# Kernel optimization log

Measured on AMD Instinct MI355X. Metric: run time of the kernel, lower is better.

The kernel has to match this reference:

```python
import jax, jax.numpy as jnp
import numpy as np

B, N, C, H = 2, 384, 256, 4
D = C // H


def setup_inputs() -> dict:
    key = jax.random.key(0)
    k1, k2 = jax.random.split(key)
    x = jax.random.normal(k1, (B, N, C), dtype=jnp.float32)
    # nn.Linear(dim, 8*dim, bias=False) weight, scaled like default torch init magnitude
    W = jax.random.normal(k2, (8 * C, C), dtype=jnp.float32) / np.float32(np.sqrt(C))
    return {"x": x, "W": W}


def reference(x, W):
    Bx, Nx, Cx = x.shape
    Hh = H
    Dd = Cx // Hh
    scale = Dd ** -0.5
    # w(x): [B,N,8C] -> [B,N,8,H,D] -> [8,B,H,N,D]
    w = (x @ W.T).reshape(Bx, Nx, 8, Hh, Dd).transpose(2, 0, 3, 1, 4)
    a, b, c = w[0], w[1], w[2]          # w[3..5] (d,e,f) are unused in the torch forward
    v1, v2 = w[6], w[7]
    # pairwise logits, each [B,H,N,N]
    eAB = jnp.exp(jnp.einsum('bhid,bhjd->bhij', a, b) * scale)  # indexed [i,j]
    eCD = jnp.exp(jnp.einsum('bhid,bhjd->bhij', b, c) * scale)  # indexed [i,k]
    eEF = jnp.exp(jnp.einsum('bhid,bhjd->bhij', c, a) * scale)  # indexed [j,k]
    # exact factorization of exp(AB[ij]+CD[ik]+EF[jk]):
    # num[i,d] = sum_j eAB[ij] v1[jd] * (sum_k eCD[ik] eEF[jk] v2[kd])
    T = eEF[..., None] * v2[:, :, None, :, :]                   # [B,H,j,k,D]
    R = jnp.einsum('bhik,bhjkd->bhijd', eCD, T)                 # [B,H,i,j,D]
    num = jnp.einsum('bhij,bhjd,bhijd->bhid', eAB, v1, R)       # [B,H,N,D]
    den = jnp.sum(eAB * jnp.einsum('bhik,bhjk->bhij', eCD, eEF), axis=-1)  # [B,H,N]
    out = num / den[..., None]
    # [B,H,N,D] -> [B,N,H,D] -> [B,N,C]
    return out.transpose(0, 2, 1, 3).reshape(Bx, Nx, Cx)
```

## Files before the change

kernel.cpp:

```cpp
#include <hip/hip_runtime.h>
#include <math.h>

#define B_  2
#define N_  384
#define C_  256
#define H_  4
#define D_  64
#define NBH (B_*H_)
#define TSZ (NBH*N_*D_)
#define ESZ (NBH*N_*N_)
#define SCALE 0.125f

typedef _Float16 f16;
typedef f16  f16x8 __attribute__((ext_vector_type(8)));
typedef f16  f16x4 __attribute__((ext_vector_type(4)));
typedef float f32x4 __attribute__((ext_vector_type(4)));

__global__ __launch_bounds__(256) void proj_kernel(const float* __restrict__ x,
                                                   const float* __restrict__ W,
                                                   float* __restrict__ proj) {
    __shared__ float Xs[32][68];
    __shared__ float Ws[32][68];
    const int tid = threadIdx.x;
    const int tx = tid & 15, ty = tid >> 4;
    const int m0 = blockIdx.x * 64;
    const int c0 = blockIdx.y * 64;
    const int t  = c0 >> 8;
    const int wbase = ((t >= 3) ? (t + 3) : t) * 256;

    float acc[4][4] = {{0.f}};
    for (int k0 = 0; k0 < 256; k0 += 32) {
        __syncthreads();
#pragma unroll
        for (int l = 0; l < 8; ++l) {
            const int idx = l * 256 + tid;
            const int mi = idx >> 5, kk = idx & 31;
            Xs[kk][mi] = x[(m0 + mi) * 256 + k0 + kk];
            const int rem = (c0 + mi) & 255;
            Ws[kk][mi] = W[(wbase + rem) * 256 + k0 + kk];
        }
        __syncthreads();
#pragma unroll
        for (int kk = 0; kk < 32; ++kk) {
            const float4 xf = *(const float4*)&Xs[kk][ty * 4];
            const float4 wf = *(const float4*)&Ws[kk][tx * 4];
            const float xa[4] = {xf.x, xf.y, xf.z, xf.w};
            const float wa[4] = {wf.x, wf.y, wf.z, wf.w};
#pragma unroll
            for (int q = 0; q < 4; ++q)
#pragma unroll
                for (int p = 0; p < 4; ++p)
                    acc[q][p] += xa[q] * wa[p];
        }
    }
#pragma unroll
    for (int q = 0; q < 4; ++q) {
        const int r = m0 + ty * 4 + q;
        const int b = r / N_;
        const int n = r - b * N_;
#pragma unroll
        for (int p = 0; p < 4; ++p) {
            const int rem = (c0 + tx * 4 + p) & 255;
            const int h = rem >> 6, d = rem & 63;
            proj[t * TSZ + ((b * H_ + h) * N_ + n) * D_ + d] = acc[q][p];
        }
    }
}

__global__ __launch_bounds__(256) void logits_kernel(const float* __restrict__ proj,
                                                     f16* __restrict__ eabt16,
                                                     f16* __restrict__ ecd16,
                                                     f16* __restrict__ eef16) {
    __shared__ float Xs[32][68];
    __shared__ float Ys[32][68];
    const int tid = threadIdx.x;
    const int tx = tid & 15, ty = tid >> 4;
    const int i0 = blockIdx.x * 64, j0 = blockIdx.y * 64;
    const int q  = blockIdx.z >> 3;
    const int bh = blockIdx.z & 7;
    const int xt = q;
    const int yt = (q == 2) ? 0 : (q + 1);
    const float* Xp = proj + xt * TSZ + bh * N_ * D_;
    const float* Yp = proj + yt * TSZ + bh * N_ * D_;

    float acc[4][4] = {{0.f}};
    for (int k0 = 0; k0 < 64; k0 += 32) {
        __syncthreads();
#pragma unroll
        for (int l = 0; l < 8; ++l) {
            const int idx = l * 256 + tid;
            const int mi = idx >> 5, kk = idx & 31;
            Xs[kk][mi] = Xp[(i0 + mi) * 64 + k0 + kk];
            Ys[kk][mi] = Yp[(j0 + mi) * 64 + k0 + kk];
        }
        __syncthreads();
#pragma unroll
        for (int kk = 0; kk < 32; ++kk) {
            const float4 xf = *(const float4*)&Xs[kk][ty * 4];
            const float4 yf = *(const float4*)&Ys[kk][tx * 4];
            const float xa[4] = {xf.x, xf.y, xf.z, xf.w};
            const float ya[4] = {yf.x, yf.y, yf.z, yf.w};
#pragma unroll
            for (int qq = 0; qq < 4; ++qq)
#pragma unroll
                for (int p = 0; p < 4; ++p)
                    acc[qq][p] += xa[qq] * ya[p];
        }
    }
#pragma unroll
    for (int qq = 0; qq < 4; ++qq)
#pragma unroll
        for (int p = 0; p < 4; ++p) {
            const float e = expf(acc[qq][p] * SCALE);
            const int ii = i0 + ty * 4 + qq;
            const int jj = j0 + tx * 4 + p;
            if (q == 0)      eabt16[(size_t)bh * N_ * N_ + jj * N_ + ii] = (f16)e;
            else if (q == 1) ecd16 [(size_t)bh * N_ * N_ + ii * N_ + jj] = (f16)e;
            else             eef16 [(size_t)bh * N_ * N_ + ii * N_ + jj] = (f16)e;
        }
}

__global__ __launch_bounds__(256) void triplet_mfma2_kernel(
        const f16*  __restrict__ eabt,
        const f16*  __restrict__ ecdh,
        const f16*  __restrict__ eefh,
        const float* __restrict__ v1,
        const float* __restrict__ v2,
        float* __restrict__ numout) {
    __shared__ __align__(16) f16 eefs[64 * 384];
    __shared__ __align__(16) f16 v2s[4 * 384];

    const int tid  = threadIdx.x;
    const int lane = tid & 63;
    const int w    = tid >> 6;
    const int quad = lane >> 4;
    const int lr   = lane & 15;
    const int j0 = blockIdx.x * 64;
    const int dg = blockIdx.y;
    const int bh = blockIdx.z;
    const int dd = dg * 4 + w;

    const f16*   eabtb = eabt + (size_t)bh * N_ * N_;
    const f16*   ecdb  = ecdh + (size_t)bh * N_ * N_;
    const f16*   eefb  = eefh + (size_t)bh * N_ * N_;
    const float* v1b   = v1 + (size_t)bh * N_ * D_;
    const float* v2b   = v2 + (size_t)bh * N_ * D_;

    {
        const int row = tid >> 2;
#pragma unroll
        for (int rep = 0; rep < 12; ++rep) {
            const int kb = (tid & 3) + rep * 4;
            *(uint4*)(eefs + row * 384 + ((kb ^ (row & 7)) << 3)) =
                *(const uint4*)(eefb + (j0 + row) * N_ + kb * 8);
        }
    }
#pragma unroll
    for (int rep = 0; rep < 6; ++rep) {
        const int id = rep * 256 + tid;
        const int c = id / 384, k = id - c * 384;
        const int d2 = dg * 4 + c;
        v2s[c * 384 + k] = (f16)((d2 < 64) ? v2b[k * 64 + d2] : 1.0f);
    }
    float v1r[4];
#pragma unroll
    for (int js = 0; js < 4; ++js)
        v1r[js] = (dd < 64) ? v1b[(j0 + js * 16 + lr) * 64 + dd] : 1.0f;
    __syncthreads();

    const int swzbase = lr & 7;

    for (int it = 0; it < 6; ++it) {
        const int i0 = it * 64;
        __syncthreads();

        f32x4 acc[4][4];
#pragma unroll
        for (int a = 0; a < 4; ++a)
#pragma unroll
            for (int b = 0; b < 4; ++b)
                acc[a][b] = (f32x4){0.f, 0.f, 0.f, 0.f};

        f16x8 pf[4];
#pragma unroll
        for (int isub = 0; isub < 4; ++isub)
            pf[isub] = *(const f16x8*)(ecdb + (i0 + isub * 16 + lr) * N_ + quad * 8);

        for (int ks = 0; ks < 12; ++ks) {
            const f16x8 v2f = *(const f16x8*)(v2s + w * 384 + ks * 32 + quad * 8);
            f16x8 af[4];
#pragma unroll
            for (int isub = 0; isub < 4; ++isub)
                af[isub] = pf[isub] * v2f;
            if (ks < 11) {
#pragma unroll
                for (int isub = 0; isub < 4; ++isub)
                    pf[isub] = *(const f16x8*)(ecdb + (i0 + isub * 16 + lr) * N_ +
                                               (ks + 1) * 32 + quad * 8);
            }
#pragma unroll
            for (int js = 0; js < 4; ++js) {
                const f16x8 bf = *(const f16x8*)(eefs + (js * 16 + lr) * 384 +
                                                 (((ks * 4 + quad) ^ swzbase) << 3));
#pragma unroll
                for (int isub = 0; isub < 4; ++isub)
                    acc[isub][js] = __builtin_amdgcn_mfma_f32_16x16x32_f16(
                        af[isub], bf, acc[isub][js], 0, 0, 0);
            }
        }
        float numacc[16];
#pragma unroll
        for (int r = 0; r < 16; ++r) numacc[r] = 0.f;
#pragma unroll
        for (int js = 0; js < 4; ++js)
#pragma unroll
            for (int isub = 0; isub < 4; ++isub) {
                const f16x4 ab = *(const f16x4*)(eabtb + (j0 + js * 16 + lr) * N_ +
                                                 i0 + isub * 16 + quad * 4);
#pragma unroll
                for (int q = 0; q < 4; ++q)
                    numacc[isub * 4 + q] += (float)ab[q] * (v1r[js] * acc[isub][js][q]);
            }
#pragma unroll
        for (int r = 0; r < 16; ++r) {
            float v = numacc[r];
            v += __shfl_xor(v, 1);
            v += __shfl_xor(v, 2);
            v += __shfl_xor(v, 4);
            v += __shfl_xor(v, 8);
            numacc[r] = v;
        }
        if (lr == 0 && dd <= 64) {
#pragma unroll
            for (int r = 0; r < 16; ++r) {
                const int i = i0 + (r >> 2) * 16 + quad * 4 + (r & 3);
                atomicAdd(&numout[((size_t)bh * N_ + i) * 68 + dd], numacc[r]);
            }
        }
    }
}

__global__ __launch_bounds__(256) void finalize_kernel(const float* __restrict__ numw,
                                                       float* __restrict__ out) {
    const int o = blockIdx.x * 256 + threadIdx.x;
    const int b = o / (N_ * C_);
    const int rem = o - b * (N_ * C_);
    const int n = rem >> 8;
    const int cc = rem & 255;
    const int h = cc >> 6, d = cc & 63;
    const float* base = numw + (((size_t)b * H_ + h) * N_ + n) * 68;
    out[o] = base[d] / base[64];
}

extern "C" void kernel_launch(void* const* d_in, const int* in_sizes, int n_in,
                              void* d_out, int out_size, void* d_ws, size_t ws_size,
                              hipStream_t stream) {
    const float* x = (const float*)d_in[0];
    const float* W = (const float*)d_in[1];
    float* ws    = (float*)d_ws;
    float* proj  = ws;
    float* numw  = ws + 5 * TSZ;
    f16*   eabt  = (f16*)(numw + NBH * N_ * 68);
    f16*   eefh  = eabt + ESZ;
    f16*   ecdh  = eefh + ESZ;

    proj_kernel<<<dim3(12, 20), 256, 0, stream>>>(x, W, proj);
    logits_kernel<<<dim3(6, 6, 24), 256, 0, stream>>>(proj, eabt, ecdh, eefh);
    hipMemsetAsync(numw, 0, (size_t)NBH * N_ * 68 * sizeof(float), stream);
    triplet_mfma2_kernel<<<dim3(6, 17, 8), 256, 0, stream>>>(
        eabt, ecdh, eefh, proj + 3 * TSZ, proj + 4 * TSZ, numw);
    finalize_kernel<<<dim3(768), 256, 0, stream>>>(numw, (float*)d_out);
}
```

Before: 289.5 us.

## Keep eCD/eEF tiles in registers and loop over d per block

Reworks the triplet kernel so each block holds its 64x384 eCD and eEF fragments in registers and iterates over up to 36 d-columns, instead of reloading eEF into shared memory for every d-group. A new transpose kernel converts v1/v2 to f16 in a d-major layout, so v2 rows load with vector copies. Per-j-tile partial sums are written to separate buffers and summed in finalize, which removes the memset and the global atomics. The cost is very high register pressure (96 f16x8 fragments per thread, launch bounds set to one block), fewer blocks overall, and an extra kernel launch.

```diff
diff --git a/kernel.cpp b/kernel.cpp
--- a/kernel.cpp
+++ b/kernel.cpp
@@ -120,59 +120,92 @@
         }
 }
 
-__global__ __launch_bounds__(256) void triplet_mfma2_kernel(
-        const f16*  __restrict__ eabt,
-        const f16*  __restrict__ ecdh,
-        const f16*  __restrict__ eefh,
-        const float* __restrict__ v1,
-        const float* __restrict__ v2,
-        float* __restrict__ numout) {
-    __shared__ __align__(16) f16 eefs[64 * 384];
-    __shared__ __align__(16) f16 v2s[4 * 384];
+__global__ __launch_bounds__(256) void vtrans_kernel(const float* __restrict__ proj,
+                                                     f16* __restrict__ vt) {
+    __shared__ f16 tile[64][65];
+    const int tid = threadIdx.x;
+    const int n0 = blockIdx.x * 64;
+    const int bh = blockIdx.y;
+    const int t  = blockIdx.z;
+    const float* src = proj + (3 + t) * TSZ + ((size_t)bh * N_ + n0) * 64;
+#pragma unroll
+    for (int rep = 0; rep < 16; ++rep) {
+        const int idx = rep * 256 + tid;
+        const int r = idx >> 6, d = idx & 63;
+        tile[d][r] = (f16)src[r * 64 + d];
+    }
+    __syncthreads();
+#pragma unroll
+    for (int rep = 0; rep < 16; ++rep) {
+        const int idx = rep * 256 + tid;
+        const int d = idx >> 6, c = idx & 63;
+        vt[((size_t)(t * NBH + bh) * 64 + d) * N_ + n0 + c] = tile[d][c];
+    }
+}
+
+__global__ __launch_bounds__(256, 1) void triplet_reg_kernel(
+        const f16* __restrict__ eabt,
+        const f16* __restrict__ ecdh,
+        const f16* __restrict__ eefh,
+        const f16* __restrict__ vt,
+        float* __restrict__ numw6) {
+    __shared__ __align__(16) f16 v2s[36 * 384];
 
     const int tid  = threadIdx.x;
     const int lane = tid & 63;
     const int w    = tid >> 6;
     const int quad = lane >> 4;
     const int lr   = lane & 15;
-    const int j0 = blockIdx.x * 64;
-    const int dg = blockIdx.y;
-    const int bh = blockIdx.z;
-    const int dd = dg * 4 + w;
-
-    const f16*   eabtb = eabt + (size_t)bh * N_ * N_;
-    const f16*   ecdb  = ecdh + (size_t)bh * N_ * N_;
-    const f16*   eefb  = eefh + (size_t)bh * N_ * N_;
-    const float* v1b   = v1 + (size_t)bh * N_ * D_;
-    const float* v2b   = v2 + (size_t)bh * N_ * D_;
+    const int i0 = blockIdx.x * 64;
+    const int jt = blockIdx.y;
+    const int j0 = jt * 64;
+    const int bh = blockIdx.z >> 1;
+    const int dh = blockIdx.z & 1;
+
+    const f16* eabtb = eabt + (size_t)bh * N_ * N_;
+    const f16* ecdb  = ecdh + (size_t)bh * N_ * N_;
+    const f16* eefb  = eefh + (size_t)bh * N_ * N_;
+    const f16* v1tb  = vt + (size_t)bh * 64 * N_;
+    const f16* v2tb  = vt + (size_t)(NBH + bh) * 64 * N_;
 
     {
-        const int row = tid >> 2;
-#pragma unroll
-        for (int rep = 0; rep < 12; ++rep) {
-            const int kb = (tid & 3) + rep * 4;
-            *(uint4*)(eefs + row * 384 + ((kb ^ (row & 7)) << 3)) =
-                *(const uint4*)(eefb + (j0 + row) * N_ + kb * 8);
-        }
-    }
-#pragma unroll
-    for (int rep = 0; rep < 6; ++rep) {
-        const int id = rep * 256 + tid;
-        const int c = id / 384, k = id - c * 384;
-        const int d2 = dg * 4 + c;
-        v2s[c * 384 + k] = (f16)((d2 < 64) ? v2b[k * 64 + d2] : 1.0f);
-    }
-    float v1r[4];
+#pragma unroll
+        for (int rep = 0; rep < 7; ++rep) {
+            const int idx = rep * 256 + tid;
+            if (idx < 1728) {
+                const int s = idx / 48, c = idx - s * 48;
+                const int d = dh * 36 + s;
+                if (d < 64) {
+                    *(uint4*)(v2s + s * 384 + c * 8) =
+                        *(const uint4*)(v2tb + (size_t)d * N_ + c * 8);
+                } else {
+                    f16x8 one = {1, 1, 1, 1, 1, 1, 1, 1};
+                    *(f16x8*)(v2s + s * 384 + c * 8) = one;
+                }
+            }
+        }
+    }
+
+    f16x8 cf[4][12];
+    f16x8 bf[4][12];
+#pragma unroll
+    for (int isub = 0; isub < 4; ++isub)
+#pragma unroll
+        for (int ks = 0; ks < 12; ++ks)
+            cf[isub][ks] = *(const f16x8*)(ecdb + (size_t)(i0 + isub * 16 + lr) * N_ +
+                                           ks * 32 + quad * 8);
 #pragma unroll
     for (int js = 0; js < 4; ++js)
-        v1r[js] = (dd < 64) ? v1b[(j0 + js * 16 + lr) * 64 + dd] : 1.0f;
+#pragma unroll
+        for (int ks = 0; ks < 12; ++ks)
+            bf[js][ks] = *(const f16x8*)(eefb + (size_t)(j0 + js * 16 + lr) * N_ +
+                                         ks * 32 + quad * 8);
     __syncthreads();
 
-    const int swzbase = lr & 7;
-
-    for (int it = 0; it < 6; ++it) {
-        const int i0 = it * 64;
-        __syncthreads();
+    for (int t = 0; t < 9; ++t) {
+        const int s  = w * 9 + t;
+        const int dd = dh * 36 + s;
+        if (dd > 64) break;
 
         f32x4 acc[4][4];
 #pragma unroll
@@ -181,46 +214,37 @@
             for (int b = 0; b < 4; ++b)
                 acc[a][b] = (f32x4){0.f, 0.f, 0.f, 0.f};
 
-        f16x8 pf[4];
-#pragma unroll
-        for (int isub = 0; isub < 4; ++isub)
-            pf[isub] = *(const f16x8*)(ecdb + (i0 + isub * 16 + lr) * N_ + quad * 8);
-
+#pragma unroll
         for (int ks = 0; ks < 12; ++ks) {
-            const f16x8 v2f = *(const f16x8*)(v2s + w * 384 + ks * 32 + quad * 8);
+            const f16x8 v2f = *(const f16x8*)(v2s + s * 384 + ks * 32 + quad * 8);
             f16x8 af[4];
 #pragma unroll
             for (int isub = 0; isub < 4; ++isub)
-                af[isub] = pf[isub] * v2f;
-            if (ks < 11) {
-#pragma unroll
-                for (int isub = 0; isub < 4; ++isub)
-                    pf[isub] = *(const f16x8*)(ecdb + (i0 + isub * 16 + lr) * N_ +
-                                               (ks + 1) * 32 + quad * 8);
-            }
-#pragma unroll
-            for (int js = 0; js < 4; ++js) {
-                const f16x8 bf = *(const f16x8*)(eefs + (js * 16 + lr) * 384 +
-                                                 (((ks * 4 + quad) ^ swzbase) << 3));
+                af[isub] = cf[isub][ks] * v2f;
+#pragma unroll
+            for (int js = 0; js < 4; ++js)
 #pragma unroll
                 for (int isub = 0; isub < 4; ++isub)
                     acc[isub][js] = __builtin_amdgcn_mfma_f32_16x16x32_f16(
-                        af[isub], bf, acc[isub][js], 0, 0, 0);
+                        af[isub], bf[js][ks], acc[isub][js], 0, 0, 0);
+        }
+
+        float numacc[16];
+#pragma unroll
+        for (int r = 0; r < 16; ++r) numacc[r] = 0.f;
+#pragma unroll
+        for (int js = 0; js < 4; ++js) {
+            const float v1v = (dd < 64) ? (float)v1tb[(size_t)dd * N_ + j0 + js * 16 + lr]
+                                        : 1.0f;
+#pragma unroll
+            for (int isub = 0; isub < 4; ++isub) {
+                const f16x4 ab = *(const f16x4*)(eabtb + (size_t)(j0 + js * 16 + lr) * N_ +
+                                                 i0 + isub * 16 + quad * 4);
+#pragma unroll
+                for (int q = 0; q < 4; ++q)
+                    numacc[isub * 4 + q] += (float)ab[q] * (v1v * acc[isub][js][q]);
             }
         }
-        float numacc[16];
-#pragma unroll
-        for (int r = 0; r < 16; ++r) numacc[r] = 0.f;
-#pragma unroll
-        for (int js = 0; js < 4; ++js)
-#pragma unroll
-            for (int isub = 0; isub < 4; ++isub) {
-                const f16x4 ab = *(const f16x4*)(eabtb + (j0 + js * 16 + lr) * N_ +
-                                                 i0 + isub * 16 + quad * 4);
-#pragma unroll
-                for (int q = 0; q < 4; ++q)
-                    numacc[isub * 4 + q] += (float)ab[q] * (v1r[js] * acc[isub][js][q]);
-            }
 #pragma unroll
         for (int r = 0; r < 16; ++r) {
             float v = numacc[r];
@@ -230,17 +254,17 @@
             v += __shfl_xor(v, 8);
             numacc[r] = v;
         }
-        if (lr == 0 && dd <= 64) {
+        if (lr == 0) {
 #pragma unroll
             for (int r = 0; r < 16; ++r) {
                 const int i = i0 + (r >> 2) * 16 + quad * 4 + (r & 3);
-                atomicAdd(&numout[((size_t)bh * N_ + i) * 68 + dd], numacc[r]);
+                numw6[((size_t)(jt * NBH + bh) * N_ + i) * 68 + dd] = numacc[r];
             }
         }
     }
 }
 
-__global__ __launch_bounds__(256) void finalize_kernel(const float* __restrict__ numw,
+__global__ __launch_bounds__(256) void finalize_kernel(const float* __restrict__ numw6,
                                                        float* __restrict__ out) {
     const int o = blockIdx.x * 256 + threadIdx.x;
     const int b = o / (N_ * C_);
@@ -248,8 +272,15 @@
     const int n = rem >> 8;
     const int cc = rem & 255;
     const int h = cc >> 6, d = cc & 63;
-    const float* base = numw + (((size_t)b * H_ + h) * N_ + n) * 68;
-    out[o] = base[d] / base[64];
+    const size_t base = (size_t)((b * H_ + h) * N_ + n) * 68;
+    float num = 0.f, den = 0.f;
+#pragma unroll
+    for (int jt = 0; jt < 6; ++jt) {
+        const float* p = numw6 + (size_t)jt * NBH * N_ * 68 + base;
+        num += p[d];
+        den += p[64];
+    }
+    out[o] = num / den;
 }
 
 extern "C" void kernel_launch(void* const* d_in, const int* in_sizes, int n_in,
@@ -259,15 +290,15 @@
     const float* W = (const float*)d_in[1];
     float* ws    = (float*)d_ws;
     float* proj  = ws;
-    float* numw  = ws + 5 * TSZ;
-    f16*   eabt  = (f16*)(numw + NBH * N_ * 68);
+    float* numw6 = ws + 5 * TSZ;
+    f16*   eabt  = (f16*)(numw6 + 6 * NBH * N_ * 68);
     f16*   eefh  = eabt + ESZ;
     f16*   ecdh  = eefh + ESZ;
+    f16*   vt    = ecdh + ESZ;
 
     proj_kernel<<<dim3(12, 20), 256, 0, stream>>>(x, W, proj);
     logits_kernel<<<dim3(6, 6, 24), 256, 0, stream>>>(proj, eabt, ecdh, eefh);
-    hipMemsetAsync(numw, 0, (size_t)NBH * N_ * 68 * sizeof(float), stream);
-    triplet_mfma2_kernel<<<dim3(6, 17, 8), 256, 0, stream>>>(
-        eabt, ecdh, eefh, proj + 3 * TSZ, proj + 4 * TSZ, numw);
-    finalize_kernel<<<dim3(768), 256, 0, stream>>>(numw, (float*)d_out);
-}
+    vtrans_kernel<<<dim3(6, 8, 2), 256, 0, stream>>>(proj, vt);
+    triplet_reg_kernel<<<dim3(6, 6, 16), 256, 0, stream>>>(eabt, ecdh, eefh, vt, numw6);
+    finalize_kernel<<<dim3(768), 256, 0, stream>>>(numw6, (float*)d_out);
+}
```

Result: slower. 325.8 us (+12.6%).
